# Performance work log

Measured on AMD Instinct MI355X. Metric: run time of the kernel, lower is better.

The kernel has to match this reference:

```python
import jax, jax.numpy as jnp
import numpy as np

B, TQ, TKV, NPR, H, D = 4, 1024, 1024, 5, 16, 64
IN, OUT, R, P, NT = 1024, H * D, 64, 4096, 4
KV = NPR + TKV  # prompt tokens prepended to kv sequence


def setup_inputs() -> dict:
    key = jax.random.key(0)
    ks = jax.random.split(key, 20)
    n = lambda k, shp, s: jax.random.normal(k, shp, jnp.float32) * s
    W = 0.02  # weight init scale
    return {
        "pe": n(ks[0], (P, OUT), 1.0),
        "attn_output": n(ks[1], (B, TQ, OUT), 1.0),
        "q": n(ks[2], (B, H, TQ, D), 1.0),
        "kv_query": n(ks[3], (B, TKV, IN), 1.0),
        "attn_mask": jnp.zeros((TQ, KV), jnp.float32),
        "prompt": n(ks[4], (NT, NPR, IN), 1.0),
        "gates": n(ks[5], (1,), 1.0),
        "k_w1": n(ks[6], (IN, R), W), "k_w2": n(ks[7], (R, OUT), W),
        "v_w1": n(ks[8], (IN, R), W), "v_w2": n(ks[9], (R, OUT), W),
        "kp_w1": n(ks[10], (OUT, R), W), "kp_w2": n(ks[11], (R, OUT), W),
        "qp_w1": n(ks[12], (OUT, R), W), "qp_w2": n(ks[13], (R, OUT), W),
        "indices_a": jax.random.randint(ks[14], (B, TQ), 0, P),
        "indices_b": jax.random.randint(ks[15], (B, TKV), 0, P),
        "task_idx": jax.random.randint(ks[16], (B,), 0, NT),
    }


def reference(pe, attn_output, q, kv_query, attn_mask, prompt, gates,
              k_w1, k_w2, v_w1, v_w2, kp_w1, kp_w2, qp_w1, qp_w2,
              indices_a, indices_b, task_idx):
    # prompt selection + concat in front of kv sequence
    pr = prompt[task_idx]                                   # [B, NPR, IN]
    kv_x = jnp.concatenate([pr, kv_query], axis=1)          # [B, KV, IN]
    # positional features; key_pos is zero-padded over the prompt slots
    key_pos = jnp.pad(pe[indices_b], ((0, 0), (NPR, 0), (0, 0)))  # [B, KV, OUT]
    # low-rank projections
    k = (kv_x @ k_w1) @ k_w2 + (key_pos @ kp_w1) @ kp_w2    # [B, KV, OUT]
    v = (kv_x @ v_w1) @ v_w2                                # [B, KV, OUT]
    q_pos = (pe[indices_a] @ qp_w1) @ qp_w2                 # [B, TQ, OUT]
    qh = q + q_pos.reshape(B, TQ, H, D).transpose(0, 2, 1, 3)
    kh = k.reshape(B, KV, H, D).transpose(0, 2, 1, 3)
    vh = v.reshape(B, KV, H, D).transpose(0, 2, 1, 3)
    scores = jnp.einsum('bhqd,bhkd->bhqk', qh, kh) / np.float32(np.sqrt(D))
    scores = scores + attn_mask[None, None]                 # 2D mask path
    w = jax.nn.softmax(scores, axis=-1)                     # dropout = identity (eval)
    out = jnp.einsum('bhqk,bhkd->bhqd', w, vh)
    out = out.transpose(0, 2, 1, 3).reshape(B, TQ, OUT)
    return out * gates + attn_output
```

## Files before the change

kernel.cpp:

```cpp
#include <hip/hip_runtime.h>
#include <hip/hip_bf16.h>

#define B_    4
#define TQ_   1024
#define TKV_  1024
#define NPR_  5
#define H_    16
#define D_    64
#define IN_   1024
#define OUT_  1024
#define R_    64
#define KV_   1029
#define KVP_  1088
#define M1_   4116
#define M1P_  4160
#define MQ_   4096
#define NKT_  17
#define NQT_  16
#define LOG2E_ 1.4426950408889634f
#define SQ_SCALE_ (0.125f * 1.4426950408889634f)

typedef __attribute__((ext_vector_type(8))) short short8;
typedef __attribute__((ext_vector_type(4))) float f32x4;
typedef __attribute__((ext_vector_type(4))) unsigned uint4v;
typedef __attribute__((ext_vector_type(2))) unsigned uint2v;

#define MFMA(a, b, c) __builtin_amdgcn_mfma_f32_16x16x32_bf16(a, b, c, 0, 0, 0)

#define AS1 __attribute__((address_space(1)))
#define AS3 __attribute__((address_space(3)))
#define GLDS(g, l) __builtin_amdgcn_global_load_lds((const AS1 void*)(g), (AS3 void*)(l), 16, 0, 0)

static __device__ __forceinline__ short f2bf(float f) {
  unsigned u = __builtin_bit_cast(unsigned, f);
  u += 0x7fffu + ((u >> 16) & 1u);
  return (short)(u >> 16);
}

static __device__ __forceinline__ short8 zero8() {
  short8 z = {0, 0, 0, 0, 0, 0, 0, 0};
  return z;
}

static __device__ __forceinline__ unsigned cvtpk(float lo, float hi) {
  unsigned r;
  asm("v_cvt_pk_bf16_f32 %0, %1, %2" : "=v"(r) : "v"(lo), "v"(hi));
  return r;
}
static __device__ __forceinline__ void pl32(unsigned &a, unsigned &b) {
  asm("v_permlane32_swap_b32 %0, %1" : "+v"(a), "+v"(b));
}
static __device__ __forceinline__ void pl16(unsigned &a, unsigned &b) {
  asm("v_permlane16_swap_b32 %0, %1" : "+v"(a), "+v"(b));
}
static __device__ __forceinline__ float redmax4(float x) {
  unsigned a = __builtin_bit_cast(unsigned, x), b = a;
  pl16(a, b);
  x = fmaxf(__builtin_bit_cast(float, a), __builtin_bit_cast(float, b));
  a = b = __builtin_bit_cast(unsigned, x);
  pl32(a, b);
  return fmaxf(__builtin_bit_cast(float, a), __builtin_bit_cast(float, b));
}
static __device__ __forceinline__ float redsum4(float x) {
  unsigned a = __builtin_bit_cast(unsigned, x), b = a;
  pl16(a, b);
  x = __builtin_bit_cast(float, a) + __builtin_bit_cast(float, b);
  a = b = __builtin_bit_cast(unsigned, x);
  pl32(a, b);
  return __builtin_bit_cast(float, a) + __builtin_bit_cast(float, b);
}
static __device__ __forceinline__ f32x4 vmax4(f32x4 a, f32x4 b) {
  f32x4 r;
  r[0] = fmaxf(a[0], b[0]); r[1] = fmaxf(a[1], b[1]);
  r[2] = fmaxf(a[2], b[2]); r[3] = fmaxf(a[3], b[3]);
  return r;
}
static __device__ __forceinline__ void cd2bfrag(const f32x4 (&s)[4], short8 &p0, short8 &p1) {
  unsigned u00 = cvtpk(s[0][0], s[0][1]), u01 = cvtpk(s[0][2], s[0][3]);
  unsigned u10 = cvtpk(s[1][0], s[1][1]), u11 = cvtpk(s[1][2], s[1][3]);
  unsigned u20 = cvtpk(s[2][0], s[2][1]), u21 = cvtpk(s[2][2], s[2][3]);
  unsigned u30 = cvtpk(s[3][0], s[3][1]), u31 = cvtpk(s[3][2], s[3][3]);
  pl32(u00, u10); pl32(u01, u11); pl32(u20, u30); pl32(u21, u31);
  pl16(u00, u10); pl16(u01, u11); pl16(u20, u30); pl16(u21, u31);
  uint4v w0 = {u00, u01, u10, u11};
  uint4v w1 = {u20, u21, u30, u31};
  p0 = __builtin_bit_cast(short8, w0);
  p1 = __builtin_bit_cast(short8, w1);
}

__global__ __launch_bounds__(256) void prep(
    const float* __restrict__ kw1, const float* __restrict__ vw1,
    const float* __restrict__ kpw1, const float* __restrict__ qpw1,
    const float* __restrict__ kw2, const float* __restrict__ vw2,
    const float* __restrict__ kpw2, const float* __restrict__ qpw2,
    const float* __restrict__ mask,
    short* __restrict__ w1t, short* __restrict__ w2t, int* __restrict__ mflags) {
  int bid = blockIdx.x;
  if (bid < 64) {
    int tid = bid * 256 + threadIdx.x;
    const float* w1s[4] = {kw1, vw1, kpw1, qpw1};
    const float* w2s[4] = {kw2, vw2, kpw2, qpw2};
    for (int i = tid; i < 4 * R_ * IN_; i += 64 * 256) {
      int m = i >> 16, p = i & 65535, r = p >> 10, k = p & 1023;
      w1t[i] = f2bf(w1s[m][k * R_ + r]);
    }
    for (int i = tid; i < 4 * OUT_ * R_; i += 64 * 256) {
      int m = i >> 16, p = i & 65535, o = p >> 6, r = p & 63;
      w2t[i] = f2bf(w2s[m][r * OUT_ + o]);
    }
  } else {
    int t = bid - 64;
    int qt = t / NKT_, kt = t % NKT_;
    int nz = 0;
    for (int it = 0; it < 16; ++it) {
      int e = it * 256 + threadIdx.x;
      int rr = e >> 6, cc = e & 63;
      int kv = kt * 64 + cc;
      if (kv < KV_) {
        float v = mask[(size_t)(qt * 64 + rr) * KV_ + kv];
        nz |= (v != 0.0f);
      }
    }
    __shared__ int snz[4];
    unsigned long long bv = __ballot(nz);
    if ((threadIdx.x & 63) == 0) snz[threadIdx.x >> 6] = (bv != 0ULL);
    __syncthreads();
    if (threadIdx.x == 0) mflags[t] = snz[0] | snz[1] | snz[2] | snz[3];
  }
}

__global__ __launch_bounds__(256) void stage1(
    const float* __restrict__ prompt, const float* __restrict__ kv_query,
    const float* __restrict__ pe, const int* __restrict__ indices_a,
    const int* __restrict__ indices_b, const int* __restrict__ task_idx,
    const short* __restrict__ w1t, float* __restrict__ part) {
  int which = blockIdx.z;
  int chunk = blockIdx.y;
  int mbase = blockIdx.x * 64;
  int lane = threadIdx.x & 63, wave = threadIdx.x >> 6;
  int lrow = lane & 15, lg = lane >> 4;
  int row = mbase + wave * 16 + lrow;

  const float* asrc = nullptr;
  if (which == 0) {
    int r = min(row, M1_ - 1);
    int b = r / KV_, t = r - b * KV_;
    asrc = (t < NPR_) ? prompt + (size_t)(task_idx[b] * NPR_ + t) * IN_
                      : kv_query + (size_t)(b * TKV_ + t - NPR_) * IN_;
  } else if (which == 1) {
    int r = min(row, M1_ - 1);
    int b = r / KV_, t = r - b * KV_;
    if (t >= NPR_) asrc = pe + (size_t)indices_b[b * TKV_ + t - NPR_] * OUT_;
  } else {
    int r = min(row, MQ_ - 1);
    asrc = pe + (size_t)indices_a[r] * OUT_;
  }
  const short* bt0 = w1t + (size_t)((which == 0) ? 0 : (which == 1) ? 2 : 3) * (R_ * IN_);
  const short* bt1 = w1t + (size_t)1 * (R_ * IN_);
  int k0base = chunk * 256;

  f32x4 acc0[4], acc1[4];
#pragma unroll
  for (int f = 0; f < 4; ++f) { acc0[f] = (f32x4){0,0,0,0}; acc1[f] = (f32x4){0,0,0,0}; }

#pragma unroll
  for (int ks = 0; ks < 8; ++ks) {
    int kc = k0base + ks * 32 + lg * 8;
    short8 a;
    if (asrc) {
      f32x4 a0 = *(const f32x4*)(asrc + kc);
      f32x4 a1 = *(const f32x4*)(asrc + kc + 4);
      uint4v au = {cvtpk(a0[0], a0[1]), cvtpk(a0[2], a0[3]),
                   cvtpk(a1[0], a1[1]), cvtpk(a1[2], a1[3])};
      a = __builtin_bit_cast(short8, au);
    } else {
      a = zero8();
    }
#pragma unroll
    for (int f = 0; f < 4; ++f) {
      short8 b0 = *(const short8*)(bt0 + (size_t)(f * 16 + lrow) * IN_ + kc);
      acc0[f] = MFMA(a, b0, acc0[f]);
      if (which == 0) {
        short8 b1 = *(const short8*)(bt1 + (size_t)(f * 16 + lrow) * IN_ + kc);
        acc1[f] = MFMA(a, b1, acc1[f]);
      }
    }
  }
  int o0 = (which == 0) ? 0 : (which == 1) ? 2 : 3;
  float* p0 = part + (size_t)(o0 * 4 + chunk) * (M1P_ * R_);
#pragma unroll
  for (int f = 0; f < 4; ++f)
#pragma unroll
    for (int r = 0; r < 4; ++r)
      p0[(size_t)(mbase + wave * 16 + lg * 4 + r) * R_ + f * 16 + lrow] = acc0[f][r];
  if (which == 0) {
    float* p1 = part + (size_t)(1 * 4 + chunk) * (M1P_ * R_);
#pragma unroll
    for (int f = 0; f < 4; ++f)
#pragma unroll
      for (int r = 0; r < 4; ++r)
        p1[(size_t)(mbase + wave * 16 + lg * 4 + r) * R_ + f * 16 + lrow] = acc1[f][r];
  }
}

__global__ __launch_bounds__(256) void reduce1(const float* __restrict__ part,
                                               short* __restrict__ tall) {
  int tid = blockIdx.x * 256 + threadIdx.x;
  int o = tid / 66560;
  int idx = (tid - o * 66560) * 4;
  const float* p = part + (size_t)(o * 4) * (M1P_ * R_) + idx;
  f32x4 v0 = *(const f32x4*)(p);
  f32x4 v1 = *(const f32x4*)(p + (size_t)(M1P_ * R_));
  f32x4 v2 = *(const f32x4*)(p + (size_t)2 * (M1P_ * R_));
  f32x4 v3 = *(const f32x4*)(p + (size_t)3 * (M1P_ * R_));
  f32x4 s = (v0 + v1) + (v2 + v3);
  uint2v w = {cvtpk(s[0], s[1]), cvtpk(s[2], s[3])};
  *(uint2v*)(tall + (size_t)o * (M1P_ * R_) + idx) = w;
}

__global__ __launch_bounds__(256) void stage2(
    const short* __restrict__ tall, const short* __restrict__ w2t,
    short* __restrict__ kbf, short* __restrict__ vtb) {
  int z = blockIdx.z;
  int lane = threadIdx.x & 63, wave = threadIdx.x >> 6;
  int lrow = lane & 15, lg = lane >> 4;
  const short* tk  = tall;
  const short* tv  = tall + (size_t)1 * (M1P_ * R_);
  const short* tkp = tall + (size_t)2 * (M1P_ * R_);

  f32x4 acc[4];
#pragma unroll
  for (int f = 0; f < 4; ++f) acc[f] = (f32x4){0,0,0,0};

  if (z == 0) {
    int mt = blockIdx.x;
    int nbase = blockIdx.y * 64;
    int arow = mt * 64 + wave * 16 + lrow;
    int b = arow / KVP_, kv = arow - b * KVP_;
    bool valid = (kv < KV_);
    const short* ta = valid ? tk  + (size_t)(b * KV_ + kv) * R_ : nullptr;
    const short* tb = valid ? tkp + (size_t)(b * KV_ + kv) * R_ : nullptr;
    const short* w2k  = w2t;
    const short* w2kp = w2t + (size_t)2 * (OUT_ * R_);
#pragma unroll
    for (int ks = 0; ks < 2; ++ks) {
      int kc = ks * 32 + lg * 8;
      short8 a1 = ta ? *(const short8*)(ta + kc) : zero8();
      short8 a2 = tb ? *(const short8*)(tb + kc) : zero8();
#pragma unroll
      for (int f = 0; f < 4; ++f) {
        int col = nbase + f * 16 + lrow;
        acc[f] = MFMA(a1, *(const short8*)(w2k  + (size_t)col * R_ + kc), acc[f]);
        acc[f] = MFMA(a2, *(const short8*)(w2kp + (size_t)col * R_ + kc), acc[f]);
      }
    }
#pragma unroll
    for (int f = 0; f < 4; ++f)
#pragma unroll
      for (int r = 0; r < 4; ++r) {
        int orow = mt * 64 + wave * 16 + lg * 4 + r;
        int ob = orow / KVP_, okv = orow - ob * KVP_;
        int kt = okv >> 6, rin = okv & 63;
        int o = nbase + f * 16 + lrow;
        int h = o >> 6, d = o & 63;
        float val = (okv < KV_) ? acc[f][r] : 0.f;
        kbf[((size_t)((ob * H_ + h) * NKT_ + kt) << 12) + rin * 64 + (d ^ ((rin & 7) << 3))] = f2bf(val);
      }
  } else {
    int cb = blockIdx.x;
    int obase = blockIdx.y * 64;
    int aorow = obase + wave * 16 + lrow;
    const short* w2v = w2t + (size_t)1 * (OUT_ * R_);
#pragma unroll
    for (int ks = 0; ks < 2; ++ks) {
      int kc = ks * 32 + lg * 8;
      short8 a = *(const short8*)(w2v + (size_t)aorow * R_ + kc);
#pragma unroll
      for (int f = 0; f < 4; ++f) {
        int crow = cb * 64 + f * 16 + lrow;
        int b = crow / KVP_, kv = crow - b * KVP_;
        short8 bfr = (kv < KV_) ? *(const short8*)(tv + (size_t)(b * KV_ + kv) * R_ + kc)
                                : zero8();
        acc[f] = MFMA(a, bfr, acc[f]);
      }
    }
#pragma unroll
    for (int f = 0; f < 4; ++f)
#pragma unroll
      for (int r = 0; r < 4; ++r) {
        int o = obase + wave * 16 + lg * 4 + r;
        int h = o >> 6, d = o & 63;
        int crow = cb * 64 + f * 16 + lrow;
        int b = crow / KVP_, kv = crow - b * KVP_;
        int kt = kv >> 6, kvin = kv & 63;
        float val = (kv < KV_) ? acc[f][r] : 0.f;
        vtb[((size_t)((b * H_ + h) * NKT_ + kt) << 12) + d * 64 + (kvin ^ ((d & 7) << 3))] = f2bf(val);
      }
  }
}

__global__ __launch_bounds__(256, 4) void attn(
    const short* __restrict__ tall, const short* __restrict__ w2t,
    const float* __restrict__ qin,
    const short* __restrict__ kbf, const short* __restrict__ vtb,
    const float* __restrict__ mask, const int* __restrict__ mflags,
    const float* __restrict__ gates, const float* __restrict__ attn_in,
    float* __restrict__ out) {
  int bid = blockIdx.x;
  int xcd = bid & 7, wg = bid >> 3;
  int qt = wg & 15, g = wg >> 4;
  int grp = xcd * 8 + g;
  int h = grp & 15, b = grp >> 4;

  int lane = threadIdx.x & 63, wave = threadIdx.x >> 6;
  int lrow = lane & 15, lg = lane >> 4;
  int qbase = qt * 64 + wave * 16;

  __shared__ __align__(16) short kvls[2][2][4096];

  const short* ktile = kbf + ((size_t)grp * NKT_ << 12);
  const short* vtile = vtb + ((size_t)grp * NKT_ << 12);

  auto stage = [&](int kt, int bsel) {
    const short* ks = ktile + ((size_t)kt << 12) + wave * 512 + lane * 8;
    const short* vs = vtile + ((size_t)kt << 12) + wave * 512 + lane * 8;
    GLDS(ks,        &kvls[bsel][0][wave * 512]);
    GLDS(ks + 2048, &kvls[bsel][0][wave * 512 + 2048]);
    GLDS(vs,        &kvls[bsel][1][wave * 512]);
    GLDS(vs + 2048, &kvls[bsel][1][wave * 512 + 2048]);
  };

  stage(0, 0);

  short8 qa0, qa1;
  {
    const short* w2q = w2t + (size_t)3 * (OUT_ * R_);
    const short* tqp = tall + (size_t)3 * (M1P_ * R_);
    f32x4 qs[4];
#pragma unroll
    for (int f = 0; f < 4; ++f) qs[f] = (f32x4){0,0,0,0};
#pragma unroll
    for (int ks = 0; ks < 2; ++ks) {
      short8 tqf = *(const short8*)(tqp + (size_t)(b * TQ_ + qbase + lrow) * R_ + ks * 32 + lg * 8);
#pragma unroll
      for (int f = 0; f < 4; ++f) {
        short8 wf = *(const short8*)(w2q + (size_t)(h * 64 + f * 16 + lrow) * R_ + ks * 32 + lg * 8);
        qs[f] = MFMA(wf, tqf, qs[f]);
      }
    }
    const float* qrow = qin + (size_t)(b * TQ_ + qbase + lrow) * OUT_ + h * 64;
#pragma unroll
    for (int f = 0; f < 4; ++f) {
      f32x4 qv = *(const f32x4*)(qrow + f * 16 + lg * 4);
#pragma unroll
      for (int r = 0; r < 4; ++r) qs[f][r] = (qs[f][r] + qv[r]) * SQ_SCALE_;
    }
    cd2bfrag(qs, qa0, qa1);
  }

  f32x4 oacc[4];
#pragma unroll
  for (int f = 0; f < 4; ++f) oacc[f] = (f32x4){0,0,0,0};
  float mrow = -1e30f, lsum = 0.f;

  asm volatile("s_waitcnt vmcnt(0)" ::: "memory");
  __builtin_amdgcn_sched_barrier(0);
  __builtin_amdgcn_s_barrier();
  __builtin_amdgcn_sched_barrier(0);

  for (int t = 0; t < NKT_; ++t) {
    int buf = t & 1;
    if (t < NKT_ - 1) {
      stage(t + 1, buf ^ 1);
      asm volatile("s_waitcnt vmcnt(4)" ::: "memory");
    } else {
      asm volatile("s_waitcnt vmcnt(0)" ::: "memory");
    }
    __builtin_amdgcn_sched_barrier(0);
    __builtin_amdgcn_s_barrier();
    __builtin_amdgcn_sched_barrier(0);

    const short* kb = &kvls[buf][0][0];
    const short* vb = &kvls[buf][1][0];
    short8 kf[8];
#pragma unroll
    for (int f = 0; f < 4; ++f) {
      int row = f * 16 + lrow, sw = (row & 7) << 3;
      kf[f * 2 + 0] = *(const short8*)(kb + row * 64 + ((lg * 8) ^ sw));
      kf[f * 2 + 1] = *(const short8*)(kb + row * 64 + ((32 + lg * 8) ^ sw));
    }
    f32x4 s[4];
#pragma unroll
    for (int f = 0; f < 4; ++f) {
      s[f] = (f32x4){0,0,0,0};
      s[f] = MFMA(kf[f * 2 + 0], qa0, s[f]);
      s[f] = MFMA(kf[f * 2 + 1], qa1, s[f]);
    }
    short8 vf[8];
#pragma unroll
    for (int f = 0; f < 4; ++f) {
      int row = f * 16 + lrow, sw = (row & 7) << 3;
      vf[f * 2 + 0] = *(const short8*)(vb + row * 64 + ((lg * 8) ^ sw));
      vf[f * 2 + 1] = *(const short8*)(vb + row * 64 + ((32 + lg * 8) ^ sw));
    }
    int kvb = t * 64;
    if (mflags[qt * NKT_ + t]) {
      const float* mrp = mask + (size_t)(qbase + lrow) * KV_;
#pragma unroll
      for (int f = 0; f < 4; ++f)
#pragma unroll
        for (int r = 0; r < 4; ++r) {
          int kv = kvb + f * 16 + lg * 4 + r;
          if (kv < KV_) s[f][r] += mrp[kv] * LOG2E_;
        }
    }
    if (t == NKT_ - 1) {
#pragma unroll
      for (int f = 0; f < 4; ++f)
#pragma unroll
        for (int r = 0; r < 4; ++r) {
          int kv = kvb + f * 16 + lg * 4 + r;
          if (kv >= KV_) s[f][r] = -1e30f;
        }
    }
    f32x4 m03 = vmax4(vmax4(s[0], s[1]), vmax4(s[2], s[3]));
    float mt2 = fmaxf(fmaxf(m03[0], m03[1]), fmaxf(m03[2], m03[3]));
    mt2 = redmax4(mt2);
    if (__any(mt2 > mrow + 8.0f)) {
      float nm = fmaxf(mrow, mt2);
      float fac = exp2f(mrow - nm);
      mrow = nm;
      lsum *= fac;
#pragma unroll
      for (int f = 0; f < 4; ++f)
#pragma unroll
        for (int r = 0; r < 4; ++r) oacc[f][r] *= fac;
    }
#pragma unroll
    for (int f = 0; f < 4; ++f)
#pragma unroll
      for (int r = 0; r < 4; ++r) s[f][r] = exp2f(s[f][r] - mrow);
    f32x4 st = (s[0] + s[1]) + (s[2] + s[3]);
    lsum += redsum4((st[0] + st[1]) + (st[2] + st[3]));
    short8 pb0, pb1;
    cd2bfrag(s, pb0, pb1);
#pragma unroll
    for (int f = 0; f < 4; ++f) {
      oacc[f] = MFMA(vf[f * 2 + 0], pb0, oacc[f]);
      oacc[f] = MFMA(vf[f * 2 + 1], pb1, oacc[f]);
    }
    __builtin_amdgcn_sched_barrier(0);
    __builtin_amdgcn_s_barrier();
    __builtin_amdgcn_sched_barrier(0);
  }

  float g2 = gates[0];
  float sc = g2 / lsum;
  const float* ain = attn_in + (size_t)(b * TQ_ + qbase + lrow) * OUT_ + h * 64;
  float* op = out + (size_t)(b * TQ_ + qbase + lrow) * OUT_ + h * 64;
#pragma unroll
  for (int f = 0; f < 4; ++f) {
    f32x4 av = *(const f32x4*)(ain + f * 16 + lg * 4);
    f32x4 ov;
#pragma unroll
    for (int r = 0; r < 4; ++r) ov[r] = oacc[f][r] * sc + av[r];
    *(f32x4*)(op + f * 16 + lg * 4) = ov;
  }
}

extern "C" void kernel_launch(void* const* d_in, const int* in_sizes, int n_in,
                              void* d_out, int out_size, void* d_ws, size_t ws_size,
                              hipStream_t stream) {
  const float* pe          = (const float*)d_in[0];
  const float* attn_output = (const float*)d_in[1];
  const float* q           = (const float*)d_in[2];
  const float* kv_query    = (const float*)d_in[3];
  const float* attn_mask   = (const float*)d_in[4];
  const float* prompt      = (const float*)d_in[5];
  const float* gates       = (const float*)d_in[6];
  const float* k_w1        = (const float*)d_in[7];
  const float* k_w2        = (const float*)d_in[8];
  const float* v_w1        = (const float*)d_in[9];
  const float* v_w2        = (const float*)d_in[10];
  const float* kp_w1       = (const float*)d_in[11];
  const float* kp_w2       = (const float*)d_in[12];
  const float* qp_w1       = (const float*)d_in[13];
  const float* qp_w2       = (const float*)d_in[14];
  const int* indices_a     = (const int*)d_in[15];
  const int* indices_b     = (const int*)d_in[16];
  const int* task_idx      = (const int*)d_in[17];
  float* out = (float*)d_out;

  const size_t TILEB = (size_t)64 * NKT_ * 4096;

  short* ws   = (short*)d_ws;
  short* w1t  = ws;
  short* w2t  = w1t + 4 * 65536;
  short* tall = w2t + 4 * 65536;
  short* kbf  = tall + 4 * (M1P_ * R_);
  short* vtb  = kbf + TILEB;
  int* mflags = (int*)(vtb + TILEB);
  float* part = (float*)kbf;

  hipLaunchKernelGGL(prep, dim3(64 + NQT_ * NKT_), dim3(256), 0, stream,
                     k_w1, v_w1, kp_w1, qp_w1, k_w2, v_w2, kp_w2, qp_w2,
                     attn_mask, w1t, w2t, mflags);
  hipLaunchKernelGGL(stage1, dim3(65, 4, 3), dim3(256), 0, stream,
                     prompt, kv_query, pe, indices_a, indices_b, task_idx, w1t, part);
  hipLaunchKernelGGL(reduce1, dim3(1040), dim3(256), 0, stream, part, tall);
  hipLaunchKernelGGL(stage2, dim3(68, 16, 2), dim3(256), 0, stream,
                     tall, w2t, kbf, vtb);
  hipLaunchKernelGGL(attn, dim3(1024), dim3(256), 0, stream,
                     tall, w2t, q, kbf, vtb, attn_mask, mflags, gates, attn_output, out);
}
```

Before: 119.6 us.

## Fuse split-K reduction into stage2, store partials in bf16, streamline attention loop

Stage1 now writes its split-K partial sums as bf16 instead of fp32, and the separate reduce1 kernel is removed. Stage2 sums the four partials on the fly while loading its operands, and extra blocks reduce the q-position partials for the attention kernel. Each stage2 block now computes four output column tiles from one set of reduced rows, which cuts down on re-reading the partials. The attention loop is unrolled in pairs with precomputed LDS pointers, uses raw v_exp_f32, and does the cross-lane row-sum reduction once at the end instead of every tile. This saves a launch and memory traffic, but rounding the partials to bf16 before summing costs some accuracy.

```diff
diff --git a/kernel.cpp b/kernel.cpp
--- a/kernel.cpp
+++ b/kernel.cpp
@@ -17,13 +17,13 @@
 #define MQ_   4096
 #define NKT_  17
 #define NQT_  16
+#define MR_   (M1P_ * R_)
 #define LOG2E_ 1.4426950408889634f
 #define SQ_SCALE_ (0.125f * 1.4426950408889634f)
 
 typedef __attribute__((ext_vector_type(8))) short short8;
 typedef __attribute__((ext_vector_type(4))) float f32x4;
 typedef __attribute__((ext_vector_type(4))) unsigned uint4v;
-typedef __attribute__((ext_vector_type(2))) unsigned uint2v;
 
 #define MFMA(a, b, c) __builtin_amdgcn_mfma_f32_16x16x32_bf16(a, b, c, 0, 0, 0)
 
@@ -36,22 +36,31 @@
   u += 0x7fffu + ((u >> 16) & 1u);
   return (short)(u >> 16);
 }
-
+static __device__ __forceinline__ float bf2f(unsigned short u) {
+  return __builtin_bit_cast(float, (unsigned)u << 16);
+}
 static __device__ __forceinline__ short8 zero8() {
   short8 z = {0, 0, 0, 0, 0, 0, 0, 0};
   return z;
 }
-
 static __device__ __forceinline__ unsigned cvtpk(float lo, float hi) {
   unsigned r;
   asm("v_cvt_pk_bf16_f32 %0, %1, %2" : "=v"(r) : "v"(lo), "v"(hi));
   return r;
 }
+static __device__ __forceinline__ float vexp2(float x) {
+  float r;
+  asm("v_exp_f32 %0, %1" : "=v"(r) : "v"(x));
+  return r;
+}
 static __device__ __forceinline__ void pl32(unsigned &a, unsigned &b) {
   asm("v_permlane32_swap_b32 %0, %1" : "+v"(a), "+v"(b));
 }
 static __device__ __forceinline__ void pl16(unsigned &a, unsigned &b) {
   asm("v_permlane16_swap_b32 %0, %1" : "+v"(a), "+v"(b));
+}
+static __device__ __forceinline__ float m3(float a, float b, float c) {
+  return fmaxf(fmaxf(a, b), c);
 }
 static __device__ __forceinline__ float redmax4(float x) {
   unsigned a = __builtin_bit_cast(unsigned, x), b = a;
@@ -68,12 +77,6 @@
   a = b = __builtin_bit_cast(unsigned, x);
   pl32(a, b);
   return __builtin_bit_cast(float, a) + __builtin_bit_cast(float, b);
-}
-static __device__ __forceinline__ f32x4 vmax4(f32x4 a, f32x4 b) {
-  f32x4 r;
-  r[0] = fmaxf(a[0], b[0]); r[1] = fmaxf(a[1], b[1]);
-  r[2] = fmaxf(a[2], b[2]); r[3] = fmaxf(a[3], b[3]);
-  return r;
 }
 static __device__ __forceinline__ void cd2bfrag(const f32x4 (&s)[4], short8 &p0, short8 &p1) {
   unsigned u00 = cvtpk(s[0][0], s[0][1]), u01 = cvtpk(s[0][2], s[0][3]);
@@ -86,6 +89,21 @@
   uint4v w1 = {u20, u21, u30, u31};
   p0 = __builtin_bit_cast(short8, w0);
   p1 = __builtin_bit_cast(short8, w1);
+}
+static __device__ __forceinline__ short8 sum4pack(const unsigned short* p) {
+  f32x4 lo = {0, 0, 0, 0}, hi = {0, 0, 0, 0};
+#pragma unroll
+  for (int c = 0; c < 4; ++c) {
+    short8 v = *(const short8*)(p + (size_t)c * MR_);
+#pragma unroll
+    for (int j = 0; j < 4; ++j) {
+      lo[j] += bf2f((unsigned short)v[j]);
+      hi[j] += bf2f((unsigned short)v[j + 4]);
+    }
+  }
+  uint4v u = {cvtpk(lo[0], lo[1]), cvtpk(lo[2], lo[3]),
+              cvtpk(hi[0], hi[1]), cvtpk(hi[2], hi[3])};
+  return __builtin_bit_cast(short8, u);
 }
 
 __global__ __launch_bounds__(256) void prep(
@@ -133,7 +151,7 @@
     const float* __restrict__ prompt, const float* __restrict__ kv_query,
     const float* __restrict__ pe, const int* __restrict__ indices_a,
     const int* __restrict__ indices_b, const int* __restrict__ task_idx,
-    const short* __restrict__ w1t, float* __restrict__ part) {
+    const short* __restrict__ w1t, unsigned short* __restrict__ part) {
   int which = blockIdx.z;
   int chunk = blockIdx.y;
   int mbase = blockIdx.x * 64;
@@ -187,120 +205,127 @@
     }
   }
   int o0 = (which == 0) ? 0 : (which == 1) ? 2 : 3;
-  float* p0 = part + (size_t)(o0 * 4 + chunk) * (M1P_ * R_);
+  unsigned short* p0 = part + (size_t)(o0 * 4 + chunk) * MR_;
 #pragma unroll
   for (int f = 0; f < 4; ++f)
 #pragma unroll
     for (int r = 0; r < 4; ++r)
-      p0[(size_t)(mbase + wave * 16 + lg * 4 + r) * R_ + f * 16 + lrow] = acc0[f][r];
+      p0[(size_t)(mbase + wave * 16 + lg * 4 + r) * R_ + f * 16 + lrow] = (unsigned short)f2bf(acc0[f][r]);
   if (which == 0) {
-    float* p1 = part + (size_t)(1 * 4 + chunk) * (M1P_ * R_);
+    unsigned short* p1 = part + (size_t)(1 * 4 + chunk) * MR_;
 #pragma unroll
     for (int f = 0; f < 4; ++f)
 #pragma unroll
       for (int r = 0; r < 4; ++r)
-        p1[(size_t)(mbase + wave * 16 + lg * 4 + r) * R_ + f * 16 + lrow] = acc1[f][r];
-  }
-}
-
-__global__ __launch_bounds__(256) void reduce1(const float* __restrict__ part,
-                                               short* __restrict__ tall) {
-  int tid = blockIdx.x * 256 + threadIdx.x;
-  int o = tid / 66560;
-  int idx = (tid - o * 66560) * 4;
-  const float* p = part + (size_t)(o * 4) * (M1P_ * R_) + idx;
-  f32x4 v0 = *(const f32x4*)(p);
-  f32x4 v1 = *(const f32x4*)(p + (size_t)(M1P_ * R_));
-  f32x4 v2 = *(const f32x4*)(p + (size_t)2 * (M1P_ * R_));
-  f32x4 v3 = *(const f32x4*)(p + (size_t)3 * (M1P_ * R_));
-  f32x4 s = (v0 + v1) + (v2 + v3);
-  uint2v w = {cvtpk(s[0], s[1]), cvtpk(s[2], s[3])};
-  *(uint2v*)(tall + (size_t)o * (M1P_ * R_) + idx) = w;
+        p1[(size_t)(mbase + wave * 16 + lg * 4 + r) * R_ + f * 16 + lrow] = (unsigned short)f2bf(acc1[f][r]);
+  }
 }
 
 __global__ __launch_bounds__(256) void stage2(
-    const short* __restrict__ tall, const short* __restrict__ w2t,
-    short* __restrict__ kbf, short* __restrict__ vtb) {
-  int z = blockIdx.z;
+    const unsigned short* __restrict__ part, const short* __restrict__ w2t,
+    short* __restrict__ kbf, short* __restrict__ vtb, short* __restrict__ tqs) {
+  int L = blockIdx.x;
   int lane = threadIdx.x & 63, wave = threadIdx.x >> 6;
   int lrow = lane & 15, lg = lane >> 4;
-  const short* tk  = tall;
-  const short* tv  = tall + (size_t)1 * (M1P_ * R_);
-  const short* tkp = tall + (size_t)2 * (M1P_ * R_);
-
-  f32x4 acc[4];
-#pragma unroll
-  for (int f = 0; f < 4; ++f) acc[f] = (f32x4){0,0,0,0};
-
-  if (z == 0) {
-    int mt = blockIdx.x;
-    int nbase = blockIdx.y * 64;
+
+  if (L < 272) {
+    int mt = L >> 2, nh = L & 3;
     int arow = mt * 64 + wave * 16 + lrow;
     int b = arow / KVP_, kv = arow - b * KVP_;
     bool valid = (kv < KV_);
-    const short* ta = valid ? tk  + (size_t)(b * KV_ + kv) * R_ : nullptr;
-    const short* tb = valid ? tkp + (size_t)(b * KV_ + kv) * R_ : nullptr;
+    int prow = b * KV_ + min(kv, KV_ - 1);
+    short8 a1[2], a2[2];
+#pragma unroll
+    for (int ks = 0; ks < 2; ++ks) {
+      int kc = ks * 32 + lg * 8;
+      a1[ks] = valid ? sum4pack(part + (size_t)0 * MR_ + (size_t)prow * R_ + kc) : zero8();
+      a2[ks] = valid ? sum4pack(part + (size_t)8 * MR_ + (size_t)prow * R_ + kc) : zero8();
+    }
     const short* w2k  = w2t;
     const short* w2kp = w2t + (size_t)2 * (OUT_ * R_);
 #pragma unroll
-    for (int ks = 0; ks < 2; ++ks) {
-      int kc = ks * 32 + lg * 8;
-      short8 a1 = ta ? *(const short8*)(ta + kc) : zero8();
-      short8 a2 = tb ? *(const short8*)(tb + kc) : zero8();
-#pragma unroll
-      for (int f = 0; f < 4; ++f) {
-        int col = nbase + f * 16 + lrow;
-        acc[f] = MFMA(a1, *(const short8*)(w2k  + (size_t)col * R_ + kc), acc[f]);
-        acc[f] = MFMA(a2, *(const short8*)(w2kp + (size_t)col * R_ + kc), acc[f]);
+    for (int i = 0; i < 4; ++i) {
+      int nbase = (nh * 4 + i) * 64;
+      f32x4 acc[4];
+#pragma unroll
+      for (int f = 0; f < 4; ++f) acc[f] = (f32x4){0,0,0,0};
+#pragma unroll
+      for (int ks = 0; ks < 2; ++ks) {
+        int kc = ks * 32 + lg * 8;
+#pragma unroll
+        for (int f = 0; f < 4; ++f) {
+          int col = nbase + f * 16 + lrow;
+          acc[f] = MFMA(a1[ks], *(const short8*)(w2k  + (size_t)col * R_ + kc), acc[f]);
+          acc[f] = MFMA(a2[ks], *(const short8*)(w2kp + (size_t)col * R_ + kc), acc[f]);
+        }
       }
-    }
+#pragma unroll
+      for (int f = 0; f < 4; ++f)
+#pragma unroll
+        for (int r = 0; r < 4; ++r) {
+          int orow = mt * 64 + wave * 16 + lg * 4 + r;
+          int ob = orow / KVP_, okv = orow - ob * KVP_;
+          int kt = okv >> 6, rin = okv & 63;
+          int o = nbase + f * 16 + lrow;
+          int h = o >> 6, d = o & 63;
+          float val = (okv < KV_) ? acc[f][r] : 0.f;
+          kbf[((size_t)((ob * H_ + h) * NKT_ + kt) << 12) + rin * 64 + (d ^ ((rin & 7) << 3))] = f2bf(val);
+        }
+    }
+  } else if (L < 544) {
+    int Lm = L - 272;
+    int cb = Lm >> 2, oh = Lm & 3;
+    short8 bfr[8];
 #pragma unroll
     for (int f = 0; f < 4; ++f)
 #pragma unroll
-      for (int r = 0; r < 4; ++r) {
-        int orow = mt * 64 + wave * 16 + lg * 4 + r;
-        int ob = orow / KVP_, okv = orow - ob * KVP_;
-        int kt = okv >> 6, rin = okv & 63;
-        int o = nbase + f * 16 + lrow;
-        int h = o >> 6, d = o & 63;
-        float val = (okv < KV_) ? acc[f][r] : 0.f;
-        kbf[((size_t)((ob * H_ + h) * NKT_ + kt) << 12) + rin * 64 + (d ^ ((rin & 7) << 3))] = f2bf(val);
+      for (int ks = 0; ks < 2; ++ks) {
+        int crow = cb * 64 + f * 16 + lrow;
+        int b = crow / KVP_, kvr = crow - b * KVP_;
+        bfr[f * 2 + ks] = (kvr < KV_)
+            ? sum4pack(part + (size_t)4 * MR_ + (size_t)(b * KV_ + kvr) * R_ + ks * 32 + lg * 8)
+            : zero8();
       }
+    const short* w2v = w2t + (size_t)1 * (OUT_ * R_);
+#pragma unroll
+    for (int i = 0; i < 4; ++i) {
+      int obase = (oh * 4 + i) * 64;
+      int aorow = obase + wave * 16 + lrow;
+      f32x4 acc[4];
+#pragma unroll
+      for (int f = 0; f < 4; ++f) acc[f] = (f32x4){0,0,0,0};
+#pragma unroll
+      for (int ks = 0; ks < 2; ++ks) {
+        short8 a = *(const short8*)(w2v + (size_t)aorow * R_ + ks * 32 + lg * 8);
+#pragma unroll
+        for (int f = 0; f < 4; ++f) acc[f] = MFMA(a, bfr[f * 2 + ks], acc[f]);
+      }
+#pragma unroll
+      for (int f = 0; f < 4; ++f)
+#pragma unroll
+        for (int r = 0; r < 4; ++r) {
+          int o = obase + wave * 16 + lg * 4 + r;
+          int h = o >> 6, d = o & 63;
+          int crow = cb * 64 + f * 16 + lrow;
+          int b = crow / KVP_, kvr = crow - b * KVP_;
+          int kt = kvr >> 6, kvin = kvr & 63;
+          float val = (kvr < KV_) ? acc[f][r] : 0.f;
+          vtb[((size_t)((b * H_ + h) * NKT_ + kt) << 12) + d * 64 + (kvin ^ ((d & 7) << 3))] = f2bf(val);
+        }
+    }
   } else {
-    int cb = blockIdx.x;
-    int obase = blockIdx.y * 64;
-    int aorow = obase + wave * 16 + lrow;
-    const short* w2v = w2t + (size_t)1 * (OUT_ * R_);
-#pragma unroll
-    for (int ks = 0; ks < 2; ++ks) {
-      int kc = ks * 32 + lg * 8;
-      short8 a = *(const short8*)(w2v + (size_t)aorow * R_ + kc);
-#pragma unroll
-      for (int f = 0; f < 4; ++f) {
-        int crow = cb * 64 + f * 16 + lrow;
-        int b = crow / KVP_, kv = crow - b * KVP_;
-        short8 bfr = (kv < KV_) ? *(const short8*)(tv + (size_t)(b * KV_ + kv) * R_ + kc)
-                                : zero8();
-        acc[f] = MFMA(a, bfr, acc[f]);
-      }
-    }
-#pragma unroll
-    for (int f = 0; f < 4; ++f)
-#pragma unroll
-      for (int r = 0; r < 4; ++r) {
-        int o = obase + wave * 16 + lg * 4 + r;
-        int h = o >> 6, d = o & 63;
-        int crow = cb * 64 + f * 16 + lrow;
-        int b = crow / KVP_, kv = crow - b * KVP_;
-        int kt = kv >> 6, kvin = kv & 63;
-        float val = (kv < KV_) ? acc[f][r] : 0.f;
-        vtb[((size_t)((b * H_ + h) * NKT_ + kt) << 12) + d * 64 + (kvin ^ ((d & 7) << 3))] = f2bf(val);
-      }
+    int j = L - 544;
+#pragma unroll
+    for (int it = 0; it < 8; ++it) {
+      int idx = j * 16384 + it * 2048 + threadIdx.x * 8;
+      short8 v = sum4pack(part + (size_t)12 * MR_ + idx);
+      *(short8*)(tqs + idx) = v;
+    }
   }
 }
 
 __global__ __launch_bounds__(256, 4) void attn(
-    const short* __restrict__ tall, const short* __restrict__ w2t,
+    const short* __restrict__ tqs, const short* __restrict__ w2t,
     const float* __restrict__ qin,
     const short* __restrict__ kbf, const short* __restrict__ vtb,
     const float* __restrict__ mask, const int* __restrict__ mflags,
@@ -320,10 +345,21 @@
 
   const short* ktile = kbf + ((size_t)grp * NKT_ << 12);
   const short* vtile = vtb + ((size_t)grp * NKT_ << 12);
-
-  auto stage = [&](int kt, int bsel) {
-    const short* ks = ktile + ((size_t)kt << 12) + wave * 512 + lane * 8;
-    const short* vs = vtile + ((size_t)kt << 12) + wave * 512 + lane * 8;
+  const short* kg = ktile + wave * 512 + lane * 8;
+  const short* vg = vtile + wave * 512 + lane * 8;
+
+  int sw = (lrow & 7) << 3;
+  int offA = (lg * 8) ^ sw;
+  int offB = (32 + lg * 8) ^ sw;
+  const short* p0A = &kvls[0][0][lrow * 64 + offA];
+  const short* p0B = &kvls[0][0][lrow * 64 + offB];
+  const short* p1A = &kvls[1][0][lrow * 64 + offA];
+  const short* p1B = &kvls[1][0][lrow * 64 + offB];
+  const int* mfp = mflags + qt * NKT_;
+
+  auto stage = [&](int t, int bsel) {
+    const short* ks = kg + ((size_t)t << 12);
+    const short* vs = vg + ((size_t)t << 12);
     GLDS(ks,        &kvls[bsel][0][wave * 512]);
     GLDS(ks + 2048, &kvls[bsel][0][wave * 512 + 2048]);
     GLDS(vs,        &kvls[bsel][1][wave * 512]);
@@ -335,13 +371,12 @@
   short8 qa0, qa1;
   {
     const short* w2q = w2t + (size_t)3 * (OUT_ * R_);
-    const short* tqp = tall + (size_t)3 * (M1P_ * R_);
     f32x4 qs[4];
 #pragma unroll
     for (int f = 0; f < 4; ++f) qs[f] = (f32x4){0,0,0,0};
 #pragma unroll
     for (int ks = 0; ks < 2; ++ks) {
-      short8 tqf = *(const short8*)(tqp + (size_t)(b * TQ_ + qbase + lrow) * R_ + ks * 32 + lg * 8);
+      short8 tqf = *(const short8*)(tqs + (size_t)(b * TQ_ + qbase + lrow) * R_ + ks * 32 + lg * 8);
 #pragma unroll
       for (int f = 0; f < 4; ++f) {
         short8 wf = *(const short8*)(w2q + (size_t)(h * 64 + f * 16 + lrow) * R_ + ks * 32 + lg * 8);
@@ -361,17 +396,11 @@
   f32x4 oacc[4];
 #pragma unroll
   for (int f = 0; f < 4; ++f) oacc[f] = (f32x4){0,0,0,0};
-  float mrow = -1e30f, lsum = 0.f;
-
-  asm volatile("s_waitcnt vmcnt(0)" ::: "memory");
-  __builtin_amdgcn_sched_barrier(0);
-  __builtin_amdgcn_s_barrier();
-  __builtin_amdgcn_sched_barrier(0);
-
-  for (int t = 0; t < NKT_; ++t) {
-    int buf = t & 1;
-    if (t < NKT_ - 1) {
-      stage(t + 1, buf ^ 1);
+  float mrow = -1e30f, plsum = 0.f;
+
+  auto tile = [&](int t, const short* pA, const short* pB, int nbsel, bool last) {
+    if (!last) {
+      stage(t + 1, nbsel);
       asm volatile("s_waitcnt vmcnt(4)" ::: "memory");
     } else {
       asm volatile("s_waitcnt vmcnt(0)" ::: "memory");
@@ -380,31 +409,23 @@
     __builtin_amdgcn_s_barrier();
     __builtin_amdgcn_sched_barrier(0);
 
-    const short* kb = &kvls[buf][0][0];
-    const short* vb = &kvls[buf][1][0];
-    short8 kf[8];
+    f32x4 s[4];
 #pragma unroll
     for (int f = 0; f < 4; ++f) {
-      int row = f * 16 + lrow, sw = (row & 7) << 3;
-      kf[f * 2 + 0] = *(const short8*)(kb + row * 64 + ((lg * 8) ^ sw));
-      kf[f * 2 + 1] = *(const short8*)(kb + row * 64 + ((32 + lg * 8) ^ sw));
-    }
-    f32x4 s[4];
+      short8 kA = *(const short8*)(pA + f * 1024);
+      short8 kB = *(const short8*)(pB + f * 1024);
+      s[f] = (f32x4){0,0,0,0};
+      s[f] = MFMA(kA, qa0, s[f]);
+      s[f] = MFMA(kB, qa1, s[f]);
+    }
+    short8 vfr[8];
 #pragma unroll
     for (int f = 0; f < 4; ++f) {
-      s[f] = (f32x4){0,0,0,0};
-      s[f] = MFMA(kf[f * 2 + 0], qa0, s[f]);
-      s[f] = MFMA(kf[f * 2 + 1], qa1, s[f]);
-    }
-    short8 vf[8];
-#pragma unroll
-    for (int f = 0; f < 4; ++f) {
-      int row = f * 16 + lrow, sw = (row & 7) << 3;
-      vf[f * 2 + 0] = *(const short8*)(vb + row * 64 + ((lg * 8) ^ sw));
-      vf[f * 2 + 1] = *(const short8*)(vb + row * 64 + ((32 + lg * 8) ^ sw));
-    }
-    int kvb = t * 64;
-    if (mflags[qt * NKT_ + t]) {
+      vfr[f * 2 + 0] = *(const short8*)(pA + 4096 + f * 1024);
+      vfr[f * 2 + 1] = *(const short8*)(pB + 4096 + f * 1024);
+    }
+    if (mfp[t]) {
+      int kvb = t * 64;
       const float* mrp = mask + (size_t)(qbase + lrow) * KV_;
 #pragma unroll
       for (int f = 0; f < 4; ++f)
@@ -414,23 +435,27 @@
           if (kv < KV_) s[f][r] += mrp[kv] * LOG2E_;
         }
     }
-    if (t == NKT_ - 1) {
+    if (last) {
 #pragma unroll
       for (int f = 0; f < 4; ++f)
 #pragma unroll
         for (int r = 0; r < 4; ++r) {
-          int kv = kvb + f * 16 + lg * 4 + r;
+          int kv = t * 64 + f * 16 + lg * 4 + r;
           if (kv >= KV_) s[f][r] = -1e30f;
         }
     }
-    f32x4 m03 = vmax4(vmax4(s[0], s[1]), vmax4(s[2], s[3]));
-    float mt2 = fmaxf(fmaxf(m03[0], m03[1]), fmaxf(m03[2], m03[3]));
+    float t0 = m3(s[0][0], s[0][1], s[0][2]);
+    float t1 = m3(s[0][3], s[1][0], s[1][1]);
+    float t2 = m3(s[1][2], s[1][3], s[2][0]);
+    float t3 = m3(s[2][1], s[2][2], s[2][3]);
+    float t4 = m3(s[3][0], s[3][1], s[3][2]);
+    float mt2 = fmaxf(m3(m3(t0, t1, t2), t3, t4), s[3][3]);
     mt2 = redmax4(mt2);
     if (__any(mt2 > mrow + 8.0f)) {
       float nm = fmaxf(mrow, mt2);
-      float fac = exp2f(mrow - nm);
+      float fac = vexp2(mrow - nm);
       mrow = nm;
-      lsum *= fac;
+      plsum *= fac;
 #pragma unroll
       for (int f = 0; f < 4; ++f)
 #pragma unroll
@@ -439,23 +464,30 @@
 #pragma unroll
     for (int f = 0; f < 4; ++f)
 #pragma unroll
-      for (int r = 0; r < 4; ++r) s[f][r] = exp2f(s[f][r] - mrow);
+      for (int r = 0; r < 4; ++r) s[f][r] = vexp2(s[f][r] - mrow);
     f32x4 st = (s[0] + s[1]) + (s[2] + s[3]);
-    lsum += redsum4((st[0] + st[1]) + (st[2] + st[3]));
+    plsum += (st[0] + st[1]) + (st[2] + st[3]);
     short8 pb0, pb1;
     cd2bfrag(s, pb0, pb1);
 #pragma unroll
     for (int f = 0; f < 4; ++f) {
-      oacc[f] = MFMA(vf[f * 2 + 0], pb0, oacc[f]);
-      oacc[f] = MFMA(vf[f * 2 + 1], pb1, oacc[f]);
+      oacc[f] = MFMA(vfr[f * 2 + 0], pb0, oacc[f]);
+      oacc[f] = MFMA(vfr[f * 2 + 1], pb1, oacc[f]);
     }
     __builtin_amdgcn_sched_barrier(0);
     __builtin_amdgcn_s_barrier();
     __builtin_amdgcn_sched_barrier(0);
-  }
-
-  float g2 = gates[0];
-  float sc = g2 / lsum;
+  };
+
+#pragma unroll 1
+  for (int i = 0; i < 8; ++i) {
+    tile(2 * i,     p0A, p0B, 1, false);
+    tile(2 * i + 1, p1A, p1B, 0, false);
+  }
+  tile(16, p0A, p0B, 1, true);
+
+  float lsum = redsum4(plsum);
+  float sc = gates[0] / lsum;
   const float* ain = attn_in + (size_t)(b * TQ_ + qbase + lrow) * OUT_ + h * 64;
   float* op = out + (size_t)(b * TQ_ + qbase + lrow) * OUT_ + h * 64;
 #pragma unroll
@@ -496,20 +528,19 @@
   short* ws   = (short*)d_ws;
   short* w1t  = ws;
   short* w2t  = w1t + 4 * 65536;
-  short* tall = w2t + 4 * 65536;
-  short* kbf  = tall + 4 * (M1P_ * R_);
+  unsigned short* part = (unsigned short*)(w2t + 4 * 65536);
+  short* tqs  = (short*)(part + (size_t)16 * MR_);
+  short* kbf  = tqs + (size_t)MQ_ * R_;
   short* vtb  = kbf + TILEB;
   int* mflags = (int*)(vtb + TILEB);
-  float* part = (float*)kbf;
 
   hipLaunchKernelGGL(prep, dim3(64 + NQT_ * NKT_), dim3(256), 0, stream,
                      k_w1, v_w1, kp_w1, qp_w1, k_w2, v_w2, kp_w2, qp_w2,
                      attn_mask, w1t, w2t, mflags);
   hipLaunchKernelGGL(stage1, dim3(65, 4, 3), dim3(256), 0, stream,
                      prompt, kv_query, pe, indices_a, indices_b, task_idx, w1t, part);
-  hipLaunchKernelGGL(reduce1, dim3(1040), dim3(256), 0, stream, part, tall);
-  hipLaunchKernelGGL(stage2, dim3(68, 16, 2), dim3(256), 0, stream,
-                     tall, w2t, kbf, vtb);
+  hipLaunchKernelGGL(stage2, dim3(560), dim3(256), 0, stream,
+                     part, w2t, kbf, vtb, tqs);
   hipLaunchKernelGGL(attn, dim3(1024), dim3(256), 0, stream,
-                     tall, w2t, q, kbf, vtb, attn_mask, mflags, gates, attn_output, out);
-}
+                     tqs, w2t, q, kbf, vtb, attn_mask, mflags, gates, attn_output, out);
+}
```

New measurement: 109.6 us. -8.3%, faster.
